# Kernel optimization log

Measured on AMD Instinct MI355X. Metric: run time of the kernel, lower is better.

The kernel has to match this reference:

```python
import jax, jax.numpy as jnp
import numpy as np

M = 0.25      # margin m
GAMMA = 64.0  # scale gamma
N, D = 8192, 128
NUM_CLASSES = 512


def setup_inputs() -> dict:
    key = jax.random.key(0)
    k1, k2 = jax.random.split(key)
    inputs = jax.random.normal(k1, (N, D), dtype=jnp.float32)
    targets = jax.random.randint(k2, (N,), 0, NUM_CLASSES, dtype=jnp.int64)
    return {"inputs": inputs, "targets": targets}


def reference(inputs, targets):
    # L2-normalize rows -> cosine similarity matrix [n, n]
    x = inputs / jnp.linalg.norm(inputs, axis=1, keepdims=True)
    sim = x @ x.T
    # positive mask: same label (includes diagonal, matching the torch code)
    mask = targets[:, None] == targets[None, :]

    Op, On = 1.0 + M, -M
    delta_p, delta_n = 1.0 - M, M

    sim_d = jax.lax.stop_gradient(sim)  # .detach() in torch
    ap = jnp.maximum(Op - sim_d, 0.0)
    an = jnp.maximum(sim_d + On, 0.0)

    logit_p = -ap * (sim - delta_p) * GAMMA
    logit_n = an * (sim - delta_n) * GAMMA

    neg_inf = jnp.float32(-jnp.inf)
    # per-row logsumexp over positives of -logit_p, over negatives of logit_n
    lp = jax.nn.logsumexp(jnp.where(mask, -logit_p, neg_inf), axis=1)
    ln = jax.nn.logsumexp(jnp.where(mask, neg_inf, logit_n), axis=1)

    return jnp.mean(jax.nn.softplus(ln + lp))
```

## Files before the change

### kernel.cpp

```cpp
#include <hip/hip_runtime.h>
#include <math.h>


#define NR    8192
#define DIMK  128
#define NT    64
#define NBLKS 416

typedef __attribute__((ext_vector_type(8))) short short8;
typedef __attribute__((ext_vector_type(4))) float f32x4;

__device__ __forceinline__ unsigned short bf16_rne(float f) {
  uint32_t u = __float_as_uint(f);
  u += 0x7FFFu + ((u >> 16) & 1u);
  return (unsigned short)(u >> 16);
}


__global__ __launch_bounds__(256) void normalize_split_kernel(
    const float* __restrict__ x, unsigned short* __restrict__ xhi,
    unsigned short* __restrict__ xlo, float* __restrict__ gP,
    float* __restrict__ gN, int* __restrict__ counter) {
  if (blockIdx.x < 32)      gP[blockIdx.x * 256 + threadIdx.x] = 0.f;
  else if (blockIdx.x < 64) gN[(blockIdx.x - 32) * 256 + threadIdx.x] = 0.f;
  if (blockIdx.x == 64 && threadIdx.x == 0) *counter = 0;

  const int wave = threadIdx.x >> 6;
  const int lane = threadIdx.x & 63;
  const int row  = blockIdx.x * 4 + wave;
  const float2 v = ((const float2*)(x + (size_t)row * DIMK))[lane];
  float ss = v.x * v.x + v.y * v.y;
  #pragma unroll
  for (int s = 1; s < 64; s <<= 1) ss += __shfl_xor(ss, s);
  const float r = rsqrtf(ss);
  const float a = v.x * r, b = v.y * r;
  const unsigned short ha = bf16_rne(a), hb = bf16_rne(b);
  const float haf = __uint_as_float((uint32_t)ha << 16);
  const float hbf = __uint_as_float((uint32_t)hb << 16);
  ushort2 hi, lo;
  hi.x = ha; hi.y = hb;
  lo.x = bf16_rne(a - haf); lo.y = bf16_rne(b - hbf);
  ((ushort2*)xhi)[(size_t)row * 64 + lane] = hi;
  ((ushort2*)xlo)[(size_t)row * 64 + lane] = lo;
}

__global__ __launch_bounds__(512, 2) void simloss_kernel(
    const unsigned short* __restrict__ xhi, const unsigned short* __restrict__ xlo,
    const int* __restrict__ tgt, float* __restrict__ gP, float* __restrict__ gN,
    int* __restrict__ counter, float* __restrict__ out) {
  __shared__ float red[512];
  __shared__ int islast;

  const int tid  = threadIdx.x;
  const int wave = tid >> 6, lane = tid & 63;
  const int wy = wave & 3, wx = wave >> 2;
  const int q = lane >> 4, mcol = lane & 15;

  const int p  = blockIdx.x / 13;
  const int b  = blockIdx.x - p * 13;
  const int n1 = NT - p;
  const int p2 = NT - 1 - p;
  const int t0 = b * 5;

  short8 Ah[2][4], Al[2][4];
  int ta[2][4];
  float rowP[2][4], rowN[2][4];

  auto loadA = [&](int bi) {
    #pragma unroll
    for (int fr = 0; fr < 2; ++fr) {
      const int r = bi * 128 + wy * 32 + fr * 16 + mcol;
      const unsigned short* gh = xhi + (size_t)r * DIMK + q * 8;
      const unsigned short* gl = xlo + (size_t)r * DIMK + q * 8;
      #pragma unroll
      for (int ks = 0; ks < 4; ++ks) {
        Ah[fr][ks] = *(const short8*)(gh + ks * 32);
        Al[fr][ks] = *(const short8*)(gl + ks * 32);
      }
      #pragma unroll
      for (int rg = 0; rg < 4; ++rg)
        ta[fr][rg] = tgt[bi * 128 + wy * 32 + fr * 16 + q * 4 + rg];
    }
  };
  auto zeroRows = [&]() {
    #pragma unroll
    for (int fr = 0; fr < 2; ++fr)
      #pragma unroll
      for (int rg = 0; rg < 4; ++rg) { rowP[fr][rg] = 0.f; rowN[fr][rg] = 0.f; }
  };
  auto flushRows = [&](int bi) {
    #pragma unroll
    for (int fr = 0; fr < 2; ++fr)
      #pragma unroll
      for (int rg = 0; rg < 4; ++rg) {
        float vp = rowP[fr][rg], vn = rowN[fr][rg];
        #pragma unroll
        for (int m = 1; m < 16; m <<= 1) {
          vp += __shfl_xor(vp, m);
          vn += __shfl_xor(vn, m);
        }
        if (mcol == 0) {
          const int row = bi * 128 + wy * 32 + fr * 16 + q * 4 + rg;
          atomicAdd(&gP[row], vp);
          atomicAdd(&gN[row], vn);
        }
      }
  };

  int cur_bi = (t0 < n1) ? p : p2;
  loadA(cur_bi);
  zeroRows();

  for (int tl = 0; tl < 5; ++tl) {
    const int ix = t0 + tl;
    const int bi = (ix < n1) ? p : p2;
    const int bj = (ix < n1) ? p + ix : p2 + (ix - n1);

    if (bi != cur_bi) {
      flushRows(cur_bi);
      zeroRows();
      cur_bi = bi;
      loadA(bi);
    }

    f32x4 acc[2][4];
    #pragma unroll
    for (int fr = 0; fr < 2; ++fr)
      #pragma unroll
      for (int fc = 0; fc < 4; ++fc)
        acc[fr][fc] = (f32x4){0.f, 0.f, 0.f, 0.f};

    #pragma unroll
    for (int ks = 0; ks < 4; ++ks) {
      short8 bh[4];
      #pragma unroll
      for (int fc = 0; fc < 4; ++fc) {
        const int rb = bj * 128 + wx * 64 + fc * 16 + mcol;
        bh[fc] = *(const short8*)(xhi + (size_t)rb * DIMK + ks * 32 + q * 8);
      }
      #pragma unroll
      for (int fc = 0; fc < 4; ++fc) {
        acc[0][fc] = __builtin_amdgcn_mfma_f32_16x16x32_bf16(Ah[0][ks], bh[fc], acc[0][fc], 0, 0, 0);
        acc[1][fc] = __builtin_amdgcn_mfma_f32_16x16x32_bf16(Ah[1][ks], bh[fc], acc[1][fc], 0, 0, 0);
        acc[0][fc] = __builtin_amdgcn_mfma_f32_16x16x32_bf16(Al[0][ks], bh[fc], acc[0][fc], 0, 0, 0);
        acc[1][fc] = __builtin_amdgcn_mfma_f32_16x16x32_bf16(Al[1][ks], bh[fc], acc[1][fc], 0, 0, 0);
      }
    }

    int tb[4];
    #pragma unroll
    for (int fc = 0; fc < 4; ++fc)
      tb[fc] = tgt[bj * 128 + wx * 64 + fc * 16 + mcol];

    float cP[4] = {0.f, 0.f, 0.f, 0.f}, cN[4] = {0.f, 0.f, 0.f, 0.f};
    #pragma unroll
    for (int fr = 0; fr < 2; ++fr) {
      #pragma unroll
      for (int rg = 0; rg < 4; ++rg) {
        const int taa = ta[fr][rg];
        float vp = 0.f, vn = 0.f;
        #pragma unroll
        for (int fc = 0; fc < 4; ++fc) {
          const float s  = acc[fr][fc][rg];
          const bool pos = (taa == tb[fc]);
          const float ap = fmaxf(1.25f - s, 0.f);
          const float an = fmaxf(s - 0.25f, 0.f);
          const float arg = pos ? ap * fmaf(s, 64.f, -48.f) : an * an * 64.f;
          const float e = __expf(arg);
          const float ep = pos ? e : 0.f;
          const float en = pos ? 0.f : e;
          vp += ep; vn += en;
          cP[fc] += ep; cN[fc] += en;
        }
        rowP[fr][rg] += vp;
        rowN[fr][rg] += vn;
      }
    }

    if (bj != bi) {
      #pragma unroll
      for (int fc = 0; fc < 4; ++fc) {
        float a = cP[fc], bb = cN[fc];
        a  += __shfl_xor(a, 16);  a  += __shfl_xor(a, 32);
        bb += __shfl_xor(bb, 16); bb += __shfl_xor(bb, 32);
        if (q == 0) {
          const int col = bj * 128 + wx * 64 + fc * 16 + mcol;
          atomicAdd(&gP[col], a);
          atomicAdd(&gN[col], bb);
        }
      }
    }
  }
  flushRows(cur_bi);

  __builtin_amdgcn_s_waitcnt(0);
  __syncthreads();
  if (tid == 0) islast = (atomicAdd(counter, 1) == NBLKS - 1) ? 1 : 0;
  __syncthreads();
  if (islast) {
    float local = 0.f;
    #pragma unroll 1
    for (int bb = 0; bb < 2; ++bb) {
      const int base = bb * 4096 + tid * 8;
      float pv[8], nv[8];
      #pragma unroll
      for (int u = 0; u < 8; ++u) pv[u] = atomicAdd(&gP[base + u], 0.0f);
      #pragma unroll
      for (int u = 0; u < 8; ++u) nv[u] = atomicAdd(&gN[base + u], 0.0f);
      #pragma unroll
      for (int u = 0; u < 8; ++u) local += log1pf(pv[u] * nv[u]);
    }
    red[tid] = local;
    __syncthreads();
    for (int s2 = 256; s2 > 0; s2 >>= 1) {
      if (tid < s2) red[tid] += red[tid + s2];
      __syncthreads();
    }
    if (tid == 0) out[0] = red[0] / (float)NR;
  }
}

extern "C" void kernel_launch(void* const* d_in, const int* in_sizes, int n_in,
                              void* d_out, int out_size, void* d_ws, size_t ws_size,
                              hipStream_t stream) {
  const float* x  = (const float*)d_in[0];
  const int* tgt  = (const int*)d_in[1];
  float* out      = (float*)d_out;

  unsigned short* xhi = (unsigned short*)d_ws;
  unsigned short* xlo = xhi + (size_t)NR * DIMK;
  float* gP = (float*)((char*)d_ws + (size_t)NR * DIMK * 4);
  float* gN = gP + NR;
  int* counter = (int*)(gN + NR);

  normalize_split_kernel<<<NR / 4, 256, 0, stream>>>(x, xhi, xlo, gP, gN, counter);
  simloss_kernel<<<NBLKS, 512, 0, stream>>>(xhi, xlo, tgt, gP, gN, counter, out);
}
```

Measured before the change: 134.2 us.

## Treat all pairs as negatives and correct same-class pairs in a separate kernel

The main tiled similarity kernel now computes only the negative term for every off-diagonal pair, with no label loads and no per-element positive/negative select. Two new small kernels bucket rows by class and, for each same-class pair, recompute the dot product: they add its positive exponential to gP and subtract the negative exponential that was wrongly added to gN. Per-tile column sums go through shared memory before one atomic per column, and the grid grows to 512 blocks with an uneven tile split. This trades a cheaper main loop for two extra launches, float cancellation in gN, and a per-class bucket cap of 64 rows that would silently drop pairs if a class were larger.

```diff
diff --git a/kernel.cpp b/kernel.cpp
--- a/kernel.cpp
+++ b/kernel.cpp
@@ -5,7 +5,8 @@
 #define NR    8192
 #define DIMK  128
 #define NT    64
-#define NBLKS 416
+#define NBLKS 512
+#define CCAP  64
 
 typedef __attribute__((ext_vector_type(8))) short short8;
 typedef __attribute__((ext_vector_type(4))) float f32x4;
@@ -15,15 +16,22 @@
   u += 0x7FFFu + ((u >> 16) & 1u);
   return (unsigned short)(u >> 16);
 }
+__device__ __forceinline__ float b2f(unsigned short h) {
+  return __uint_as_float((uint32_t)h << 16);
+}
 
 
 __global__ __launch_bounds__(256) void normalize_split_kernel(
     const float* __restrict__ x, unsigned short* __restrict__ xhi,
     unsigned short* __restrict__ xlo, float* __restrict__ gP,
-    float* __restrict__ gN, int* __restrict__ counter) {
+    float* __restrict__ gN, int* __restrict__ counter, int* __restrict__ cnt) {
   if (blockIdx.x < 32)      gP[blockIdx.x * 256 + threadIdx.x] = 0.f;
   else if (blockIdx.x < 64) gN[(blockIdx.x - 32) * 256 + threadIdx.x] = 0.f;
   if (blockIdx.x == 64 && threadIdx.x == 0) *counter = 0;
+  if (blockIdx.x == 65 || blockIdx.x == 66) {
+    const int c = (blockIdx.x - 65) * 256 + threadIdx.x;
+    if (c < 512) cnt[c] = 0;
+  }
 
   const int wave = threadIdx.x >> 6;
   const int lane = threadIdx.x & 63;
@@ -44,10 +52,63 @@
   ((ushort2*)xlo)[(size_t)row * 64 + lane] = lo;
 }
 
+__global__ __launch_bounds__(256) void classbuild_kernel(
+    const int* __restrict__ tgt, int* __restrict__ cnt, int* __restrict__ mem) {
+  const int row = blockIdx.x * 256 + threadIdx.x;
+  const int c = tgt[row];
+  const int idx = atomicAdd(&cnt[c], 1);
+  if (idx < CCAP) mem[c * CCAP + idx] = row;
+}
+
+__global__ __launch_bounds__(64) void positive_kernel(
+    const unsigned short* __restrict__ xhi, const unsigned short* __restrict__ xlo,
+    const int* __restrict__ cnt, const int* __restrict__ mem,
+    float* __restrict__ gP, float* __restrict__ gN) {
+  const int c = blockIdx.x;
+  const int m = min(cnt[c], CCAP);
+  const int npairs = m * m;
+  const int lane = threadIdx.x;
+  const int pr = lane >> 4, sl = lane & 15;
+  const int* cm = mem + c * CCAP;
+
+  for (int base = 0; base < npairs; base += 4) {
+    const int g = base + pr;
+    const bool valid = g < npairs;
+    const int gg = valid ? g : 0;
+    const int a  = (npairs > 0) ? cm[gg / m] : 0;
+    const int b  = (npairs > 0) ? cm[gg % m] : 0;
+    const int o1 = ((a >> 7) <= (b >> 7)) ? a : b;
+    const int o2 = ((a >> 7) <= (b >> 7)) ? b : a;
+
+    const short8 h1 = *(const short8*)(xhi + (size_t)o1 * DIMK + sl * 8);
+    const short8 l1 = *(const short8*)(xlo + (size_t)o1 * DIMK + sl * 8);
+    const short8 h2 = *(const short8*)(xhi + (size_t)o2 * DIMK + sl * 8);
+    float d = 0.f;
+    #pragma unroll
+    for (int k = 0; k < 8; ++k)
+      d += (b2f((unsigned short)h1[k]) + b2f((unsigned short)l1[k])) *
+           b2f((unsigned short)h2[k]);
+    #pragma unroll
+    for (int sh = 1; sh < 16; sh <<= 1) d += __shfl_xor(d, sh);
+
+    if (valid && sl == 0) {
+      const float s = d;
+      const float ap = fmaxf(1.25f - s, 0.f);
+      const float ep = __expf(ap * fmaf(s, 64.f, -48.f));
+      atomicAdd(&gP[a], ep);
+      if (a != b) {
+        const float t = fmaxf(fmaf(s, 8.f, -2.f), 0.f);
+        atomicAdd(&gN[a], -__expf(t * t));
+      }
+    }
+  }
+}
+
 __global__ __launch_bounds__(512, 2) void simloss_kernel(
     const unsigned short* __restrict__ xhi, const unsigned short* __restrict__ xlo,
-    const int* __restrict__ tgt, float* __restrict__ gP, float* __restrict__ gN,
+    float* __restrict__ gP, float* __restrict__ gN,
     int* __restrict__ counter, float* __restrict__ out) {
+  __shared__ float colbuf[5][4][128];
   __shared__ float red[512];
   __shared__ int islast;
 
@@ -56,16 +117,15 @@
   const int wy = wave & 3, wx = wave >> 2;
   const int q = lane >> 4, mcol = lane & 15;
 
-  const int p  = blockIdx.x / 13;
-  const int b  = blockIdx.x - p * 13;
+  const int p  = blockIdx.x >> 4;
+  const int b  = blockIdx.x & 15;
   const int n1 = NT - p;
   const int p2 = NT - 1 - p;
-  const int t0 = b * 5;
+  const int t0 = (b * (NT + 1)) >> 4;
+  const int t1 = ((b + 1) * (NT + 1)) >> 4;
+  const int ntile = t1 - t0;
 
   short8 Ah[2][4], Al[2][4];
-  int ta[2][4];
-  float rowP[2][4], rowN[2][4];
-
   auto loadA = [&](int bi) {
     #pragma unroll
     for (int fr = 0; fr < 2; ++fr) {
@@ -77,51 +137,22 @@
         Ah[fr][ks] = *(const short8*)(gh + ks * 32);
         Al[fr][ks] = *(const short8*)(gl + ks * 32);
       }
-      #pragma unroll
-      for (int rg = 0; rg < 4; ++rg)
-        ta[fr][rg] = tgt[bi * 128 + wy * 32 + fr * 16 + q * 4 + rg];
     }
   };
-  auto zeroRows = [&]() {
-    #pragma unroll
-    for (int fr = 0; fr < 2; ++fr)
-      #pragma unroll
-      for (int rg = 0; rg < 4; ++rg) { rowP[fr][rg] = 0.f; rowN[fr][rg] = 0.f; }
-  };
-  auto flushRows = [&](int bi) {
-    #pragma unroll
-    for (int fr = 0; fr < 2; ++fr)
-      #pragma unroll
-      for (int rg = 0; rg < 4; ++rg) {
-        float vp = rowP[fr][rg], vn = rowN[fr][rg];
-        #pragma unroll
-        for (int m = 1; m < 16; m <<= 1) {
-          vp += __shfl_xor(vp, m);
-          vn += __shfl_xor(vn, m);
-        }
-        if (mcol == 0) {
-          const int row = bi * 128 + wy * 32 + fr * 16 + q * 4 + rg;
-          atomicAdd(&gP[row], vp);
-          atomicAdd(&gN[row], vn);
-        }
-      }
-  };
+
+  float rowNa[2][4] = {{0.f}}, rowNb[2][4] = {{0.f}};
 
   int cur_bi = (t0 < n1) ? p : p2;
   loadA(cur_bi);
-  zeroRows();
-
-  for (int tl = 0; tl < 5; ++tl) {
+
+  for (int tl = 0; tl < ntile; ++tl) {
     const int ix = t0 + tl;
-    const int bi = (ix < n1) ? p : p2;
-    const int bj = (ix < n1) ? p + ix : p2 + (ix - n1);
-
-    if (bi != cur_bi) {
-      flushRows(cur_bi);
-      zeroRows();
-      cur_bi = bi;
-      loadA(bi);
-    }
+    const bool in1 = (ix < n1);
+    const int bi = in1 ? p : p2;
+    const int bj = in1 ? p + ix : p2 + (ix - n1);
+    const bool isdiag = in1 ? (ix == 0) : (ix == n1);
+
+    if (bi != cur_bi) { cur_bi = bi; loadA(bi); }
 
     f32x4 acc[2][4];
     #pragma unroll
@@ -129,7 +160,6 @@
       #pragma unroll
       for (int fc = 0; fc < 4; ++fc)
         acc[fr][fc] = (f32x4){0.f, 0.f, 0.f, 0.f};
-
     #pragma unroll
     for (int ks = 0; ks < 4; ++ks) {
       short8 bh[4];
@@ -147,51 +177,84 @@
       }
     }
 
-    int tb[4];
-    #pragma unroll
-    for (int fc = 0; fc < 4; ++fc)
-      tb[fc] = tgt[bj * 128 + wx * 64 + fc * 16 + mcol];
-
-    float cP[4] = {0.f, 0.f, 0.f, 0.f}, cN[4] = {0.f, 0.f, 0.f, 0.f};
-    #pragma unroll
-    for (int fr = 0; fr < 2; ++fr) {
+    float cN[4] = {0.f, 0.f, 0.f, 0.f};
+    if (!isdiag) {
+      #pragma unroll
+      for (int fr = 0; fr < 2; ++fr) {
+        #pragma unroll
+        for (int rg = 0; rg < 4; ++rg) {
+          float vn = 0.f;
+          #pragma unroll
+          for (int fc = 0; fc < 4; ++fc) {
+            const float s = acc[fr][fc][rg];
+            const float t = fmaxf(fmaf(s, 8.f, -2.f), 0.f);
+            const float e = __expf(t * t);
+            vn += e; cN[fc] += e;
+          }
+          if (in1) rowNa[fr][rg] += vn; else rowNb[fr][rg] += vn;
+        }
+      }
+    } else {
+      #pragma unroll
+      for (int fr = 0; fr < 2; ++fr) {
+        #pragma unroll
+        for (int rg = 0; rg < 4; ++rg) {
+          const int rid = wy * 32 + fr * 16 + q * 4 + rg;
+          float vn = 0.f;
+          #pragma unroll
+          for (int fc = 0; fc < 4; ++fc) {
+            const int cid = wx * 64 + fc * 16 + mcol;
+            const float s = acc[fr][fc][rg];
+            const float t = fmaxf(fmaf(s, 8.f, -2.f), 0.f);
+            float e = __expf(t * t);
+            e = (rid == cid) ? 0.f : e;
+            vn += e; cN[fc] += e;
+          }
+          if (in1) rowNa[fr][rg] += vn; else rowNb[fr][rg] += vn;
+        }
+      }
+    }
+
+    #pragma unroll
+    for (int fc = 0; fc < 4; ++fc) {
+      cN[fc] += __shfl_xor(cN[fc], 16);
+      cN[fc] += __shfl_xor(cN[fc], 32);
+    }
+    if (q == 0) {
+      #pragma unroll
+      for (int fc = 0; fc < 4; ++fc)
+        colbuf[tl][wy][wx * 64 + fc * 16 + mcol] = cN[fc];
+    }
+  }
+
+  __syncthreads();
+
+  for (int t = tid; t < ntile * 128; t += 512) {
+    const int tl = t >> 7, col = t & 127;
+    const int ix = t0 + tl;
+    const bool in1 = (ix < n1);
+    const bool dg = in1 ? (ix == 0) : (ix == n1);
+    if (!dg) {
+      const int bj = in1 ? p + ix : p2 + (ix - n1);
+      const float sum = colbuf[tl][0][col] + colbuf[tl][1][col] +
+                        colbuf[tl][2][col] + colbuf[tl][3][col];
+      atomicAdd(&gN[bj * 128 + col], sum);
+    }
+  }
+  #pragma unroll
+  for (int set = 0; set < 2; ++set) {
+    const int bi = set ? p2 : p;
+    #pragma unroll
+    for (int fr = 0; fr < 2; ++fr)
       #pragma unroll
       for (int rg = 0; rg < 4; ++rg) {
-        const int taa = ta[fr][rg];
-        float vp = 0.f, vn = 0.f;
+        float vn = set ? rowNb[fr][rg] : rowNa[fr][rg];
         #pragma unroll
-        for (int fc = 0; fc < 4; ++fc) {
-          const float s  = acc[fr][fc][rg];
-          const bool pos = (taa == tb[fc]);
-          const float ap = fmaxf(1.25f - s, 0.f);
-          const float an = fmaxf(s - 0.25f, 0.f);
-          const float arg = pos ? ap * fmaf(s, 64.f, -48.f) : an * an * 64.f;
-          const float e = __expf(arg);
-          const float ep = pos ? e : 0.f;
-          const float en = pos ? 0.f : e;
-          vp += ep; vn += en;
-          cP[fc] += ep; cN[fc] += en;
-        }
-        rowP[fr][rg] += vp;
-        rowN[fr][rg] += vn;
-      }
-    }
-
-    if (bj != bi) {
-      #pragma unroll
-      for (int fc = 0; fc < 4; ++fc) {
-        float a = cP[fc], bb = cN[fc];
-        a  += __shfl_xor(a, 16);  a  += __shfl_xor(a, 32);
-        bb += __shfl_xor(bb, 16); bb += __shfl_xor(bb, 32);
-        if (q == 0) {
-          const int col = bj * 128 + wx * 64 + fc * 16 + mcol;
-          atomicAdd(&gP[col], a);
-          atomicAdd(&gN[col], bb);
-        }
-      }
-    }
-  }
-  flushRows(cur_bi);
+        for (int m = 1; m < 16; m <<= 1) vn += __shfl_xor(vn, m);
+        if (mcol == 0)
+          atomicAdd(&gN[bi * 128 + wy * 32 + fr * 16 + q * 4 + rg], vn);
+      }
+  }
 
   __builtin_amdgcn_s_waitcnt(0);
   __syncthreads();
@@ -229,10 +292,15 @@
 
   unsigned short* xhi = (unsigned short*)d_ws;
   unsigned short* xlo = xhi + (size_t)NR * DIMK;
-  float* gP = (float*)((char*)d_ws + (size_t)NR * DIMK * 4);
+  char* base = (char*)d_ws + (size_t)NR * DIMK * 4;
+  float* gP = (float*)base;
   float* gN = gP + NR;
   int* counter = (int*)(gN + NR);
-
-  normalize_split_kernel<<<NR / 4, 256, 0, stream>>>(x, xhi, xlo, gP, gN, counter);
-  simloss_kernel<<<NBLKS, 512, 0, stream>>>(xhi, xlo, tgt, gP, gN, counter, out);
-}
+  int* cnt = counter + 16;
+  int* mem = cnt + 512;
+
+  normalize_split_kernel<<<NR / 4, 256, 0, stream>>>(x, xhi, xlo, gP, gN, counter, cnt);
+  classbuild_kernel<<<NR / 256, 256, 0, stream>>>(tgt, cnt, mem);
+  positive_kernel<<<512, 64, 0, stream>>>(xhi, xlo, cnt, mem, gP, gN);
+  simloss_kernel<<<NBLKS, 512, 0, stream>>>(xhi, xlo, gP, gN, counter, out);
+}
```

Result: slower. 276.3 us (+105.9%).
